# Kernel tuning notes

Measured on AMD Instinct MI355X. Metric: run time of the kernel, lower is better.

## Reference

```python
import jax, jax.numpy as jnp
import numpy as np

PATCH = 3
ALPHA = 0.5
EPS = 1e-12  # F.normalize default eps


def _unfold(x, p):
    # nn.Unfold(kernel_size=p, padding=p//2) then reshape(B, C, p*p, H*W)
    B, C, H, W = x.shape
    pad = p // 2
    xp = jnp.pad(x, ((0, 0), (0, 0), (pad, pad), (pad, pad)))
    # kernel positions row-major, matching torch unfold channel-major layout
    pats = jnp.stack([xp[:, :, i:i + H, j:j + W]
                      for i in range(p) for j in range(p)], axis=2)  # [B,C,K,H,W]
    return pats.reshape(B, C, p * p, H * W)


def setup_inputs() -> dict:
    key = jax.random.key(0)
    k1, k2 = jax.random.split(key)
    B, C, H, W = 4, 32, 256, 256
    fe_lv = jax.random.normal(k1, (B, C, H, W), dtype=jnp.float32)
    fused_features = jax.random.normal(k2, (B, C, H, W), dtype=jnp.float32)
    return {"fe_lv": fe_lv, "fused_features": fused_features}


def reference(fe_lv, fused_features):
    B, C, H, W = fe_lv.shape
    N = H * W
    patches = _unfold(fused_features, PATCH)          # [B,C,K,N]
    fe_flat = fe_lv.reshape(B, C, N)                  # [B,C,N]

    # cosine similarity over channel dim
    pn = patches / jnp.maximum(jnp.linalg.norm(patches, axis=1, keepdims=True), EPS)
    fn = fe_flat / jnp.maximum(jnp.linalg.norm(fe_flat, axis=1, keepdims=True), EPS)
    cosine_sim = jnp.einsum('bckn,bcn->bnk', pn, fn)  # [B,N,K]
    cosine_weights = jax.nn.softmax(cosine_sim, axis=-1)

    # euclidean distance over channel dim
    dist = jnp.sqrt(jnp.sum((patches - fe_flat[:, :, None, :]) ** 2, axis=1))  # [B,K,N]
    euclidean_weights = jax.nn.softmax(-dist.transpose(0, 2, 1), axis=-1)      # [B,N,K]

    weights = ALPHA * cosine_weights + (1.0 - ALPHA) * euclidean_weights
    refined = jnp.einsum('bnk,bckn->bcn', weights, patches)  # [B,C,N]
    return refined.reshape(B, C, H, W) + fe_lv
```

## Files before the change

### kernel.cpp

```cpp
#include <hip/hip_runtime.h>
#include <math.h>

#define B_ 4
#define C_ 32
#define H_ 256
#define W_ 256
#define HW_ (H_ * W_)
#define K_ 9
#define TX 32
#define TY 4
#define HX 34
#define HY 6
#define HCH (HX * HY)
#define NPAIR 16
#define HWORDS (HCH * NPAIR)
#define EPS_ 1e-12f

typedef _Float16 h2v __attribute__((ext_vector_type(2)));

__global__ __launch_bounds__(256, 8) void asfr_kernel(const float* __restrict__ fe,
                                                      const float* __restrict__ fu,
                                                      float* __restrict__ out) {
    __shared__ h2v smem[HWORDS];
    const int t = threadIdx.x;
    const int bx = blockIdx.x & 7;
    const int by = (blockIdx.x >> 3) & 63;
    const int b  = blockIdx.x >> 9;
    const int w0 = bx * TX, h0 = by * TY;

    const float* fub = fu + b * (C_ * HW_);
#pragma unroll 4
    for (int j = 0; j < 12; ++j) {
        int i = t + j * 256;
        int pair = i / HCH;
        int pos = i - pair * HCH;
        int r = pos / HX;
        int col = pos - r * HX;
        int hh = h0 - 1 + r;
        int ww = w0 - 1 + col;
        float a = 0.f, bb = 0.f;
        if (((unsigned)hh < (unsigned)H_) && ((unsigned)ww < (unsigned)W_)) {
            const float* p = fub + (2 * pair) * HW_ + hh * W_ + ww;
            a = p[0]; bb = p[HW_];
        }
        h2v v = {(_Float16)a, (_Float16)bb};
        smem[i] = v;
    }
    {
        int i = t + 3072;
        if (i < HWORDS) {
            int pair = i / HCH;
            int pos = i - pair * HCH;
            int r = pos / HX;
            int col = pos - r * HX;
            int hh = h0 - 1 + r;
            int ww = w0 - 1 + col;
            float a = 0.f, bb = 0.f;
            if (((unsigned)hh < (unsigned)H_) && ((unsigned)ww < (unsigned)W_)) {
                const float* p = fub + (2 * pair) * HW_ + hh * W_ + ww;
                a = p[0]; bb = p[HW_];
            }
            h2v v = {(_Float16)a, (_Float16)bb};
            smem[i] = v;
        }
    }
    __syncthreads();

    const int x = t & 31;
    const int half = (t >> 5) & 1;
    const int y = t >> 6;
    const int p0 = half << 3;
    const int pxoff = b * (C_ * HW_) + (h0 + y) * W_ + (w0 + x);
    const int hc = (y + 1) * HX + (x + 1);
    const int koff[K_] = {-HX - 1, -HX, -HX + 1, -1, 0, 1, HX - 1, HX, HX + 1};

    h2v da[K_], qa[K_];
    const h2v zz = {(_Float16)0, (_Float16)0};
#pragma unroll
    for (int k = 0; k < K_; ++k) { da[k] = zz; qa[k] = zz; }
    float fsq = 0.f;

#pragma unroll 4
    for (int pp = 0; pp < 8; ++pp) {
        const int pr = p0 + pp;
        const float* fp = fe + pxoff + (2 * pr) * HW_;
        float fa = fp[0], fb = fp[HW_];
        fsq = fmaf(fa, fa, fmaf(fb, fb, fsq));
        h2v fe2 = {(_Float16)fa, (_Float16)fb};
        const int sb = pr * HCH + hc;
#pragma unroll
        for (int k = 0; k < K_; ++k) {
            h2v p = smem[sb + koff[k]];
            da[k] += p * fe2;
            qa[k] += p * p;
        }
    }

    float dot[K_], psq[K_];
#pragma unroll
    for (int k = 0; k < K_; ++k) {
        dot[k] = (float)da[k][0] + (float)da[k][1];
        psq[k] = (float)qa[k][0] + (float)qa[k][1];
        dot[k] += __shfl_xor(dot[k], 32);
        psq[k] += __shfl_xor(psq[k], 32);
    }
    fsq += __shfl_xor(fsq, 32);

    float nf = fmaxf(sqrtf(fsq), EPS_);
    float cosv[K_], negd[K_];
#pragma unroll
    for (int k = 0; k < K_; ++k) {
        float np = fmaxf(sqrtf(psq[k]), EPS_);
        cosv[k] = __fdividef(dot[k], np * nf);
        float dsq = fmaxf(psq[k] - 2.f * dot[k] + fsq, 0.f);
        negd[k] = -sqrtf(dsq);
    }

    float m1 = cosv[0], m2 = negd[0];
#pragma unroll
    for (int k = 1; k < K_; ++k) { m1 = fmaxf(m1, cosv[k]); m2 = fmaxf(m2, negd[k]); }
    float s1 = 0.f, s2 = 0.f, e1[K_], e2[K_];
#pragma unroll
    for (int k = 0; k < K_; ++k) {
        e1[k] = __expf(cosv[k] - m1);
        e2[k] = __expf(negd[k] - m2);
        s1 += e1[k]; s2 += e2[k];
    }
    float r1 = __fdividef(0.5f, s1), r2 = __fdividef(0.5f, s2);
    h2v w2[K_];
#pragma unroll
    for (int k = 0; k < K_; ++k) {
        float wk = fmaf(e1[k], r1, e2[k] * r2);
        _Float16 wh = (_Float16)wk;
        h2v tmp = {wh, wh};
        w2[k] = tmp;
    }

#pragma unroll 2
    for (int pp = 0; pp < 8; ++pp) {
        const int pr = p0 + pp;
        const int sb = pr * HCH + hc;
        h2v acc = zz;
#pragma unroll
        for (int k = 0; k < K_; ++k) acc += w2[k] * smem[sb + koff[k]];
        const float* fp = fe + pxoff + (2 * pr) * HW_;
        float* op = out + pxoff + (2 * pr) * HW_;
        op[0]   = fp[0]   + (float)acc[0];
        op[HW_] = fp[HW_] + (float)acc[1];
    }
}

extern "C" void kernel_launch(void* const* d_in, const int* in_sizes, int n_in,
                              void* d_out, int out_size, void* d_ws, size_t ws_size,
                              hipStream_t stream) {
    const float* fe = (const float*)d_in[0];
    const float* fu = (const float*)d_in[1];
    float* out = (float*)d_out;
    dim3 grid((W_ / TX) * (H_ / TY) * B_), block(256);
    hipLaunchKernelGGL(asfr_kernel, grid, block, 0, stream, fe, fu, out);
}
```

Measured before the change: 38.23 us.

## Interleave smem channel pairs for 64-bit LDS reads, use fdot2, cache fe in registers

Rearranges the shared-memory halo so that two channel pairs for each position sit next to each other, which lets each thread fetch four fp16 channels with one 64-bit LDS load. The dot-product and squared-norm accumulations switch to the fdot2 builtin, which accumulates in fp32 instead of fp16 packed accumulators. The fe values for the thread's 16 channels are loaded once into registers before the halo fill and reused in the epilogue, so fe is no longer read twice from global memory. The costs are higher register pressure from the 16 cached floats and a changed accumulation precision.

Result: slower. 128.3 us (+235.5%).

```diff
diff --git a/kernel.cpp b/kernel.cpp
--- a/kernel.cpp
+++ b/kernel.cpp
@@ -13,20 +13,39 @@
 #define HY 6
 #define HCH (HX * HY)
 #define NPAIR 16
+#define NQUAD 8
 #define HWORDS (HCH * NPAIR)
 #define EPS_ 1e-12f
 
 typedef _Float16 h2v __attribute__((ext_vector_type(2)));
+typedef _Float16 h4v __attribute__((ext_vector_type(4)));
+
+#if defined(__has_builtin)
+#if __has_builtin(__builtin_amdgcn_fdot2)
+#define HAVE_FDOT2 1
+#endif
+#endif
 
 __global__ __launch_bounds__(256, 8) void asfr_kernel(const float* __restrict__ fe,
                                                       const float* __restrict__ fu,
                                                       float* __restrict__ out) {
     __shared__ h2v smem[HWORDS];
+    h4v* smem4 = reinterpret_cast<h4v*>(smem);
     const int t = threadIdx.x;
     const int bx = blockIdx.x & 7;
     const int by = (blockIdx.x >> 3) & 63;
     const int b  = blockIdx.x >> 9;
     const int w0 = bx * TX, h0 = by * TY;
+
+    const int x = t & 31;
+    const int half = (t >> 5) & 1;
+    const int y = t >> 6;
+    const int c0 = half << 4;
+    const int pxoff = b * (C_ * HW_) + (h0 + y) * W_ + (w0 + x);
+
+    float fereg[16];
+#pragma unroll
+    for (int cc = 0; cc < 16; ++cc) fereg[cc] = fe[pxoff + (c0 + cc) * HW_];
 
     const float* fub = fu + b * (C_ * HW_);
 #pragma unroll 4
@@ -44,7 +63,7 @@
             a = p[0]; bb = p[HW_];
         }
         h2v v = {(_Float16)a, (_Float16)bb};
-        smem[i] = v;
+        smem[(pair >> 1) * (2 * HCH) + 2 * pos + (pair & 1)] = v;
     }
     {
         int i = t + 3072;
@@ -61,46 +80,68 @@
                 a = p[0]; bb = p[HW_];
             }
             h2v v = {(_Float16)a, (_Float16)bb};
-            smem[i] = v;
+            smem[(pair >> 1) * (2 * HCH) + 2 * pos + (pair & 1)] = v;
         }
     }
     __syncthreads();
 
-    const int x = t & 31;
-    const int half = (t >> 5) & 1;
-    const int y = t >> 6;
-    const int p0 = half << 3;
-    const int pxoff = b * (C_ * HW_) + (h0 + y) * W_ + (w0 + x);
     const int hc = (y + 1) * HX + (x + 1);
     const int koff[K_] = {-HX - 1, -HX, -HX + 1, -1, 0, 1, HX - 1, HX, HX + 1};
-
+    const int q0 = half << 2;
+
+    float fsq = 0.f;
+#pragma unroll
+    for (int cc = 0; cc < 16; ++cc) fsq = fmaf(fereg[cc], fereg[cc], fsq);
+
+    h2v fe2[8];
+#pragma unroll
+    for (int pp = 0; pp < 8; ++pp) {
+        h2v v = {(_Float16)fereg[2 * pp], (_Float16)fereg[2 * pp + 1]};
+        fe2[pp] = v;
+    }
+
+    float dot[K_], psq[K_];
+#pragma unroll
+    for (int k = 0; k < K_; ++k) { dot[k] = 0.f; psq[k] = 0.f; }
+#if !defined(HAVE_FDOT2)
     h2v da[K_], qa[K_];
     const h2v zz = {(_Float16)0, (_Float16)0};
 #pragma unroll
     for (int k = 0; k < K_; ++k) { da[k] = zz; qa[k] = zz; }
-    float fsq = 0.f;
-
-#pragma unroll 4
-    for (int pp = 0; pp < 8; ++pp) {
-        const int pr = p0 + pp;
-        const float* fp = fe + pxoff + (2 * pr) * HW_;
-        float fa = fp[0], fb = fp[HW_];
-        fsq = fmaf(fa, fa, fmaf(fb, fb, fsq));
-        h2v fe2 = {(_Float16)fa, (_Float16)fb};
-        const int sb = pr * HCH + hc;
+#endif
+
+#pragma unroll
+    for (int j = 0; j < 4; ++j) {
+        const int qb = (q0 + j) * HCH + hc;
+        h2v fA = fe2[2 * j], fB = fe2[2 * j + 1];
 #pragma unroll
         for (int k = 0; k < K_; ++k) {
-            h2v p = smem[sb + koff[k]];
-            da[k] += p * fe2;
-            qa[k] += p * p;
-        }
-    }
-
-    float dot[K_], psq[K_];
+            h4v p4 = smem4[qb + koff[k]];
+            h2v pA = __builtin_shufflevector(p4, p4, 0, 1);
+            h2v pB = __builtin_shufflevector(p4, p4, 2, 3);
+#if defined(HAVE_FDOT2)
+            dot[k] = __builtin_amdgcn_fdot2(pA, fA, dot[k], false);
+            dot[k] = __builtin_amdgcn_fdot2(pB, fB, dot[k], false);
+            psq[k] = __builtin_amdgcn_fdot2(pA, pA, psq[k], false);
+            psq[k] = __builtin_amdgcn_fdot2(pB, pB, psq[k], false);
+#else
+            da[k] += pA * fA;
+            da[k] += pB * fB;
+            qa[k] += pA * pA;
+            qa[k] += pB * pB;
+#endif
+        }
+    }
+#if !defined(HAVE_FDOT2)
 #pragma unroll
     for (int k = 0; k < K_; ++k) {
         dot[k] = (float)da[k][0] + (float)da[k][1];
         psq[k] = (float)qa[k][0] + (float)qa[k][1];
+    }
+#endif
+
+#pragma unroll
+    for (int k = 0; k < K_; ++k) {
         dot[k] += __shfl_xor(dot[k], 32);
         psq[k] += __shfl_xor(psq[k], 32);
     }
@@ -136,17 +177,24 @@
         w2[k] = tmp;
     }
 
-#pragma unroll 2
-    for (int pp = 0; pp < 8; ++pp) {
-        const int pr = p0 + pp;
-        const int sb = pr * HCH + hc;
-        h2v acc = zz;
-#pragma unroll
-        for (int k = 0; k < K_; ++k) acc += w2[k] * smem[sb + koff[k]];
-        const float* fp = fe + pxoff + (2 * pr) * HW_;
-        float* op = out + pxoff + (2 * pr) * HW_;
-        op[0]   = fp[0]   + (float)acc[0];
-        op[HW_] = fp[HW_] + (float)acc[1];
+#pragma unroll
+    for (int j = 0; j < 4; ++j) {
+        const int qb = (q0 + j) * HCH + hc;
+        h2v accA = {(_Float16)0, (_Float16)0};
+        h2v accB = {(_Float16)0, (_Float16)0};
+#pragma unroll
+        for (int k = 0; k < K_; ++k) {
+            h4v p4 = smem4[qb + koff[k]];
+            h2v pA = __builtin_shufflevector(p4, p4, 0, 1);
+            h2v pB = __builtin_shufflevector(p4, p4, 2, 3);
+            accA += w2[k] * pA;
+            accB += w2[k] * pB;
+        }
+        const int cg = c0 + 4 * j;
+        out[pxoff + (cg + 0) * HW_] = fereg[4 * j + 0] + (float)accA[0];
+        out[pxoff + (cg + 1) * HW_] = fereg[4 * j + 1] + (float)accA[1];
+        out[pxoff + (cg + 2) * HW_] = fereg[4 * j + 2] + (float)accB[0];
+        out[pxoff + (cg + 3) * HW_] = fereg[4 * j + 3] + (float)accB[1];
     }
 }
 
```
